# Kernel optimization log

Hardware: AMD Instinct MI355X
Metric: run time of the kernel (lower is better)

The kernel has to match this reference:

```python
import jax, jax.numpy as jnp
import numpy as np

N, F_IN, F_OUT, K = 16384, 64, 64, 3


def setup_inputs() -> dict:
    key = jax.random.key(0)
    k1, k2, k3, k4 = jax.random.split(key, 4)
    x = jax.random.normal(k1, (N, F_IN), dtype=jnp.float32)
    # dense rescaled Laplacian; scale so repeated matmuls stay numerically tame
    L_tilde = jax.random.normal(k2, (N, N), dtype=jnp.float32) / np.float32(np.sqrt(N))
    stdv = 1.0 / np.sqrt(F_OUT)
    weights = jax.random.uniform(k3, (K + 1, F_IN, F_OUT), dtype=jnp.float32,
                                 minval=-stdv, maxval=stdv)
    bias = jax.random.uniform(k4, (F_OUT,), dtype=jnp.float32, minval=-stdv, maxval=stdv)
    return {"x": x, "L_tilde": L_tilde, "weights": weights, "bias": bias}


def reference(x, L_tilde, weights, bias):
    # Chebyshev recurrence: T0 = x, T1 = L@x, Tk = 2*L@T_{k-1} - T_{k-2}
    T_prev = x                                   # (N, F_in)
    out = T_prev @ weights[0]                    # (N, F_out)
    T_curr = L_tilde @ x
    out = out + T_curr @ weights[1]
    for k in range(2, K + 1):                    # fixed small K: python loop is fine
        T_next = 2.0 * (L_tilde @ T_curr) - T_prev
        out = out + T_next @ weights[k]
        T_prev, T_curr = T_curr, T_next
    return out + bias
```

## Files before the change

### kernel.cpp

```cpp
#include <hip/hip_runtime.h>
#include <cstddef>
#include <cstdint>

#define NN 16384
#define FF 64
#define BM 64
#define BK 64
#define SK 4
#define KQ (NN / SK)
#define NC (KQ / BK)

typedef __attribute__((ext_vector_type(8))) short bf16x8;
typedef __attribute__((ext_vector_type(4))) float f32x4;
typedef unsigned short ushort_t;

#define GLOBAL_AS __attribute__((address_space(1)))
#define LDS_AS    __attribute__((address_space(3)))

__device__ __forceinline__ void f32_split(float f, ushort_t& h, ushort_t& l) {
    unsigned u = __builtin_bit_cast(unsigned, f);
    h = (ushort_t)(u >> 16);
    float hf = __builtin_bit_cast(float, u & 0xFFFF0000u);
    float lo = f - hf;
    l = (ushort_t)(__builtin_bit_cast(unsigned, lo) >> 16);
}

__global__ __launch_bounds__(256) void convT_init(
    const float* __restrict__ X, ushort_t* __restrict__ Th,
    ushort_t* __restrict__ Tl, const float* __restrict__ W0,
    const float* __restrict__ bias, float* __restrict__ out)
{
    __shared__ float S[64][68];
    __shared__ float W[64][64];
    const int t = threadIdx.x;
    const int rb = blockIdx.x * 64;
    {
        const int row = t >> 2;
        const int c0 = (t & 3) * 16;
        const float* src = X + (size_t)(rb + row) * FF + c0;
        *(float4*)&S[row][c0 + 0]  = *(const float4*)(src + 0);
        *(float4*)&S[row][c0 + 4]  = *(const float4*)(src + 4);
        *(float4*)&S[row][c0 + 8]  = *(const float4*)(src + 8);
        *(float4*)&S[row][c0 + 12] = *(const float4*)(src + 12);
        float4* wd = (float4*)&W[0][0];
        const float4* ws = (const float4*)W0;
#pragma unroll
        for (int j = 0; j < 4; ++j) wd[t * 4 + j] = ws[t * 4 + j];
    }
    __syncthreads();
    {
        const int cc = t >> 2;
        const int r0 = (t & 3) * 16;
        ushort_t hh[16], ll[16];
#pragma unroll
        for (int i = 0; i < 16; ++i) f32_split(S[r0 + i][cc], hh[i], ll[i]);
        unsigned wh[8], wl[8];
#pragma unroll
        for (int j = 0; j < 8; ++j) {
            wh[j] = (unsigned)hh[2 * j] | ((unsigned)hh[2 * j + 1] << 16);
            wl[j] = (unsigned)ll[2 * j] | ((unsigned)ll[2 * j + 1] << 16);
        }
        const size_t o = (size_t)cc * NN + rb + r0;
        *(uint4*)(Th + o)     = make_uint4(wh[0], wh[1], wh[2], wh[3]);
        *(uint4*)(Th + o + 8) = make_uint4(wh[4], wh[5], wh[6], wh[7]);
        *(uint4*)(Tl + o)     = make_uint4(wl[0], wl[1], wl[2], wl[3]);
        *(uint4*)(Tl + o + 8) = make_uint4(wl[4], wl[5], wl[6], wl[7]);
    }
    {
        const int row0 = (t >> 3) * 2;
        const int col0 = (t & 7) * 8;
        float acc[2][8];
        const float4 b0 = *(const float4*)(bias + col0);
        const float4 b1 = *(const float4*)(bias + col0 + 4);
#pragma unroll
        for (int r = 0; r < 2; ++r) {
            acc[r][0] = b0.x; acc[r][1] = b0.y; acc[r][2] = b0.z; acc[r][3] = b0.w;
            acc[r][4] = b1.x; acc[r][5] = b1.y; acc[r][6] = b1.z; acc[r][7] = b1.w;
        }
#pragma unroll
        for (int f = 0; f < FF; ++f) {
            const float x0 = S[row0][f];
            const float x1 = S[row0 + 1][f];
            const float4 w0 = *(const float4*)&W[f][col0];
            const float4 w1 = *(const float4*)&W[f][col0 + 4];
            acc[0][0] += x0 * w0.x; acc[0][1] += x0 * w0.y;
            acc[0][2] += x0 * w0.z; acc[0][3] += x0 * w0.w;
            acc[0][4] += x0 * w1.x; acc[0][5] += x0 * w1.y;
            acc[0][6] += x0 * w1.z; acc[0][7] += x0 * w1.w;
            acc[1][0] += x1 * w0.x; acc[1][1] += x1 * w0.y;
            acc[1][2] += x1 * w0.z; acc[1][3] += x1 * w0.w;
            acc[1][4] += x1 * w1.x; acc[1][5] += x1 * w1.y;
            acc[1][6] += x1 * w1.z; acc[1][7] += x1 * w1.w;
        }
#pragma unroll
        for (int r = 0; r < 2; ++r) {
            const size_t o = (size_t)(rb + row0 + r) * FF + col0;
            float4 v0, v1;
            v0.x = acc[r][0]; v0.y = acc[r][1]; v0.z = acc[r][2]; v0.w = acc[r][3];
            v1.x = acc[r][4]; v1.y = acc[r][5]; v1.z = acc[r][6]; v1.w = acc[r][7];
            *(float4*)(out + o) = v0;
            *(float4*)(out + o + 4) = v1;
        }
    }
}

__global__ __launch_bounds__(256) void cheb_gemm_mfma(
    const float* __restrict__ L, const ushort_t* __restrict__ Th,
    const ushort_t* __restrict__ Tl, float* __restrict__ P)
{
    __shared__ ushort_t Ah[2][BM * BK];
    __shared__ ushort_t Al[2][BM * BK];
    __shared__ ushort_t Bh[2][FF * BK];
    __shared__ ushort_t Bl[2][FF * BK];

    const int tid  = threadIdx.x;
    const int lane = tid & 63;
    const int w    = tid >> 6;
    const int s    = blockIdx.x >> 8;
    const int m    = blockIdx.x & 255;
    const int row0g = m * BM;
    const int kbase = s * KQ;

    const int wm = w >> 1, wn = w & 1;
    const int frow = lane & 15;
    const int fk8  = (lane >> 4) * 8;

    const int arow = w * 4 + (lane >> 4);
    const int akq  = lane & 15;
    const int axor = (arow & 7) << 4;

    const ushort_t* Tsrc = (w & 1) ? Tl : Th;
    const int boct0 = (w >> 1) * 4;

    f32x4 acc[2][2];
#pragma unroll
    for (int i = 0; i < 2; ++i)
#pragma unroll
        for (int j = 0; j < 2; ++j) acc[i][j] = (f32x4)0.f;

    float4 va[4];

    const float* Labase = L + (size_t)(row0g + arow) * NN + kbase + akq * 4;

#define ISSUE_B(c, slot)                                                        \
    {                                                                           \
        const size_t kc = (size_t)(c) * BK;                                     \
        char* bbase = (char*)((w & 1) ? Bl[slot] : Bh[slot]);                   \
        _Pragma("unroll")                                                       \
        for (int o = 0; o < 4; ++o) {                                           \
            const int oct = boct0 + o;                                          \
            const int col = oct * 8 + (lane >> 3);                              \
            const ushort_t* g = Tsrc + (size_t)col * NN + kbase + kc            \
                                + (((lane & 7) ^ (col & 7)) * 8);               \
            __builtin_amdgcn_global_load_lds((const GLOBAL_AS void*)g,          \
                (LDS_AS void*)(bbase + oct * 1024), 16, 0, 0);                  \
        }                                                                       \
    }

#define LOAD_A(c)                                                               \
    {                                                                           \
        const float* g = Labase + (size_t)(c) * BK;                             \
        va[0] = *(const float4*)(g);                                            \
        va[1] = *(const float4*)(g + (size_t)16 * NN);                          \
        va[2] = *(const float4*)(g + (size_t)32 * NN);                          \
        va[3] = *(const float4*)(g + (size_t)48 * NN);                          \
    }

#define CONV_WRITE_A(slot)                                                      \
    {                                                                           \
        char* ahb = (char*)Ah[slot];                                            \
        char* alb = (char*)Al[slot];                                            \
        _Pragma("unroll")                                                       \
        for (int p = 0; p < 4; ++p) {                                           \
            const int r = arow + p * 16;                                        \
            ushort_t h0, h1, h2, h3, l0, l1, l2, l3;                            \
            f32_split(va[p].x, h0, l0);                                         \
            f32_split(va[p].y, h1, l1);                                         \
            f32_split(va[p].z, h2, l2);                                         \
            f32_split(va[p].w, h3, l3);                                         \
            const unsigned hi01 = (unsigned)h0 | ((unsigned)h1 << 16);          \
            const unsigned hi23 = (unsigned)h2 | ((unsigned)h3 << 16);          \
            const unsigned lo01 = (unsigned)l0 | ((unsigned)l1 << 16);          \
            const unsigned lo23 = (unsigned)l2 | ((unsigned)l3 << 16);          \
            const int byte = (r * 128 + akq * 8) ^ axor;                        \
            *(uint2*)(ahb + byte) = make_uint2(hi01, hi23);                     \
            *(uint2*)(alb + byte) = make_uint2(lo01, lo23);                     \
        }                                                                       \
    }

    ISSUE_B(0, 0)
    LOAD_A(0)
    CONV_WRITE_A(0)
    __syncthreads();

    for (int c = 0; c < NC; ++c) {
        const int slot = c & 1;
        if (c + 1 < NC) {
            ISSUE_B(c + 1, slot ^ 1)
            LOAD_A(c + 1)
        }
        {
            const char* ahb = (const char*)Ah[slot];
            const char* alb = (const char*)Al[slot];
            const char* bhb = (const char*)Bh[slot];
            const char* blb = (const char*)Bl[slot];
#pragma unroll
            for (int ks = 0; ks < 2; ++ks) {
                const int kk = ks * 32 + fk8;
                bf16x8 Afh[2], Afl[2], Bfh[2], Bfl[2];
#pragma unroll
                for (int mt = 0; mt < 2; ++mt) {
                    const int row = wm * 32 + mt * 16 + frow;
                    const int off = (row * 128 + kk * 2) ^ ((row & 7) << 4);
                    Afh[mt] = *(const bf16x8*)(ahb + off);
                    Afl[mt] = *(const bf16x8*)(alb + off);
                }
#pragma unroll
                for (int nt = 0; nt < 2; ++nt) {
                    const int col = wn * 32 + nt * 16 + frow;
                    const int off = (col * 128 + kk * 2) ^ ((col & 7) << 4);
                    Bfh[nt] = *(const bf16x8*)(bhb + off);
                    Bfl[nt] = *(const bf16x8*)(blb + off);
                }
#pragma unroll
                for (int mt = 0; mt < 2; ++mt)
#pragma unroll
                    for (int nt = 0; nt < 2; ++nt) {
                        acc[mt][nt] = __builtin_amdgcn_mfma_f32_16x16x32_bf16(
                            Afh[mt], Bfh[nt], acc[mt][nt], 0, 0, 0);
                        acc[mt][nt] = __builtin_amdgcn_mfma_f32_16x16x32_bf16(
                            Afh[mt], Bfl[nt], acc[mt][nt], 0, 0, 0);
                        acc[mt][nt] = __builtin_amdgcn_mfma_f32_16x16x32_bf16(
                            Afl[mt], Bfh[nt], acc[mt][nt], 0, 0, 0);
                    }
            }
        }
        if (c + 1 < NC) CONV_WRITE_A(slot ^ 1)
        __syncthreads();
    }

    float* Pp = P + (size_t)s * NN * FF;
#pragma unroll
    for (int mt = 0; mt < 2; ++mt)
#pragma unroll
        for (int nt = 0; nt < 2; ++nt) {
            const int row = row0g + wm * 32 + mt * 16 + (lane >> 4) * 4;
            const int col = wn * 32 + nt * 16 + frow;
#pragma unroll
            for (int r = 0; r < 4; ++r)
                Pp[(size_t)(row + r) * FF + col] = acc[mt][nt][r];
        }
#undef ISSUE_B
#undef LOAD_A
#undef CONV_WRITE_A
}

__global__ __launch_bounds__(256) void post_hop(
    const float* __restrict__ P,
    const float* __restrict__ Tsub, const float* __restrict__ Wk,
    float* __restrict__ Tstore, ushort_t* __restrict__ Thn,
    ushort_t* __restrict__ Tln, float* __restrict__ out,
    float alpha, float beta)
{
    __shared__ float ST[64][33];
    __shared__ float WK[64][64];
    const int t = threadIdx.x;
    const int rb = blockIdx.x * 32;
    const size_t M1 = (size_t)NN * FF;

    {
        float4* wd = (float4*)&WK[0][0];
        const float4* ws = (const float4*)Wk;
#pragma unroll
        for (int j = 0; j < 4; ++j) wd[t * 4 + j] = ws[t * 4 + j];
    }

    const int row = t >> 3;
    const int c0 = (t & 7) * 8;
    const size_t o = (size_t)(rb + row) * FF + c0;

    {
        float tv[8];
#pragma unroll
        for (int half = 0; half < 2; ++half) {
            const size_t oo = o + 4 * half;
            float4 a0 = *(const float4*)(P + oo);
            const float4 a1 = *(const float4*)(P + M1 + oo);
            const float4 a2 = *(const float4*)(P + 2 * M1 + oo);
            const float4 a3 = *(const float4*)(P + 3 * M1 + oo);
            a0.x += a1.x + a2.x + a3.x; a0.y += a1.y + a2.y + a3.y;
            a0.z += a1.z + a2.z + a3.z; a0.w += a1.w + a2.w + a3.w;
            tv[4 * half + 0] = alpha * a0.x; tv[4 * half + 1] = alpha * a0.y;
            tv[4 * half + 2] = alpha * a0.z; tv[4 * half + 3] = alpha * a0.w;
        }
        if (beta != 0.f) {
            const float4 s0 = *(const float4*)(Tsub + o);
            const float4 s1 = *(const float4*)(Tsub + o + 4);
            tv[0] += beta * s0.x; tv[1] += beta * s0.y;
            tv[2] += beta * s0.z; tv[3] += beta * s0.w;
            tv[4] += beta * s1.x; tv[5] += beta * s1.y;
            tv[6] += beta * s1.z; tv[7] += beta * s1.w;
        }
        if (Tstore) {
            float4 v0, v1;
            v0.x = tv[0]; v0.y = tv[1]; v0.z = tv[2]; v0.w = tv[3];
            v1.x = tv[4]; v1.y = tv[5]; v1.z = tv[6]; v1.w = tv[7];
            *(float4*)(Tstore + o) = v0;
            *(float4*)(Tstore + o + 4) = v1;
        }
#pragma unroll
        for (int j = 0; j < 8; ++j) ST[c0 + j][row] = tv[j];
    }
    __syncthreads();

    if (Thn) {
        const int f = t >> 2;
        const int r0 = (t & 3) * 8;
        ushort_t hh[8], ll[8];
#pragma unroll
        for (int i = 0; i < 8; ++i) f32_split(ST[f][r0 + i], hh[i], ll[i]);
        unsigned wh[4], wl[4];
#pragma unroll
        for (int j = 0; j < 4; ++j) {
            wh[j] = (unsigned)hh[2 * j] | ((unsigned)hh[2 * j + 1] << 16);
            wl[j] = (unsigned)ll[2 * j] | ((unsigned)ll[2 * j + 1] << 16);
        }
        const size_t ob = (size_t)f * NN + rb + r0;
        *(uint4*)(Thn + ob) = make_uint4(wh[0], wh[1], wh[2], wh[3]);
        *(uint4*)(Tln + ob) = make_uint4(wl[0], wl[1], wl[2], wl[3]);
    }

    {
        float4 a0 = *(const float4*)(out + o);
        float4 a1 = *(const float4*)(out + o + 4);
#pragma unroll
        for (int f = 0; f < FF; ++f) {
            const float sv = ST[f][row];
            const float4 w0 = *(const float4*)&WK[f][c0];
            const float4 w1 = *(const float4*)&WK[f][c0 + 4];
            a0.x += sv * w0.x; a0.y += sv * w0.y;
            a0.z += sv * w0.z; a0.w += sv * w0.w;
            a1.x += sv * w1.x; a1.y += sv * w1.y;
            a1.z += sv * w1.z; a1.w += sv * w1.w;
        }
        *(float4*)(out + o) = a0;
        *(float4*)(out + o + 4) = a1;
    }
}

extern "C" void kernel_launch(void* const* d_in, const int* in_sizes, int n_in,
                              void* d_out, int out_size, void* d_ws, size_t ws_size,
                              hipStream_t stream)
{
    const float* x    = (const float*)d_in[0];
    const float* L    = (const float*)d_in[1];
    const float* W    = (const float*)d_in[2];
    const float* bias = (const float*)d_in[3];
    float* out = (float*)d_out;

    const size_t M1 = (size_t)NN * FF;
    float* wsf = (float*)d_ws;
    float* T1 = wsf;
    float* P  = wsf + M1;
    ushort_t* ThA = (ushort_t*)(wsf + 5 * M1);
    ushort_t* TlA = ThA + M1;
    ushort_t* ThB = TlA + M1;
    ushort_t* TlB = ThB + M1;

    const dim3 gc(NN / 64), bc(256);
    const dim3 gg(SK * 256), bg(256);
    const dim3 gp(NN / 32), bp(256);

    convT_init<<<gc, bc, 0, stream>>>(x, ThA, TlA, W + 0 * FF * FF, bias, out);
    cheb_gemm_mfma<<<gg, bg, 0, stream>>>(L, ThA, TlA, P);
    post_hop<<<gp, bp, 0, stream>>>(P, x, W + 1 * FF * FF,
                                    T1, ThB, TlB, out, 1.f, 0.f);
    cheb_gemm_mfma<<<gg, bg, 0, stream>>>(L, ThB, TlB, P);
    post_hop<<<gp, bp, 0, stream>>>(P, x, W + 2 * FF * FF,
                                    nullptr, ThA, TlA, out, 2.f, -1.f);
    cheb_gemm_mfma<<<gg, bg, 0, stream>>>(L, ThA, TlA, P);
    post_hop<<<gp, bp, 0, stream>>>(P, T1, W + 3 * FF * FF,
                                    nullptr, nullptr, nullptr, out, 2.f, -1.f);
}
```

Baseline: 725.9 us.

## Halve K-tile depth to 32 and re-layout LDS swizzle for A and B

Reduces the K chunk per pipeline stage from 64 to 32, which halves LDS tiles per stage (and LDS use, possibly raising occupancy). A loads switch to two contiguous float4 per thread per row with a new 4-way XOR swizzle, B async loads are remapped to match, and the compute loop loses its inner ks loop. The cost is twice as many iterations and barriers, with fewer bytes in flight per stage to hide memory latency on this memory-bound L stream.

```diff
diff --git a/kernel.cpp b/kernel.cpp
--- a/kernel.cpp
+++ b/kernel.cpp
@@ -5,7 +5,7 @@
 #define NN 16384
 #define FF 64
 #define BM 64
-#define BK 64
+#define BK 32
 #define SK 4
 #define KQ (NN / SK)
 #define NC (KQ / BK)
@@ -123,11 +123,11 @@
 
     const int wm = w >> 1, wn = w & 1;
     const int frow = lane & 15;
-    const int fk8  = (lane >> 4) * 8;
-
-    const int arow = w * 4 + (lane >> 4);
-    const int akq  = lane & 15;
-    const int axor = (arow & 7) << 4;
+    const int fkq  = lane >> 4;
+
+    const int ar  = tid >> 2;
+    const int akq = tid & 3;
+    const int abyte = ar * 64 + ((akq ^ (ar & 3)) << 4);
 
     const ushort_t* Tsrc = (w & 1) ? Tl : Th;
     const int boct0 = (w >> 1) * 4;
@@ -138,54 +138,86 @@
 #pragma unroll
         for (int j = 0; j < 2; ++j) acc[i][j] = (f32x4)0.f;
 
-    float4 va[4];
-
-    const float* Labase = L + (size_t)(row0g + arow) * NN + kbase + akq * 4;
+    float4 va0, va1;
+
+    const float* Labase = L + (size_t)(row0g + ar) * NN + kbase + akq * 8;
 
 #define ISSUE_B(c, slot)                                                        \
     {                                                                           \
         const size_t kc = (size_t)(c) * BK;                                     \
         char* bbase = (char*)((w & 1) ? Bl[slot] : Bh[slot]);                   \
         _Pragma("unroll")                                                       \
-        for (int o = 0; o < 4; ++o) {                                           \
-            const int oct = boct0 + o;                                          \
-            const int col = oct * 8 + (lane >> 3);                              \
-            const ushort_t* g = Tsrc + (size_t)col * NN + kbase + kc            \
-                                + (((lane & 7) ^ (col & 7)) * 8);               \
+        for (int j = 0; j < 2; ++j) {                                           \
+            const int oct2 = boct0 + 2 * j;                   \
+            const int col = oct2 * 8 + (lane >> 5) * 8 + ((lane & 31) >> 2);    \
+            const int sg = (lane & 3) ^ (col & 3);                              \
+            const ushort_t* g = Tsrc + (size_t)col * NN + kbase + kc + sg * 8;  \
             __builtin_amdgcn_global_load_lds((const GLOBAL_AS void*)g,          \
-                (LDS_AS void*)(bbase + oct * 1024), 16, 0, 0);                  \
+                (LDS_AS void*)(bbase + oct2 * 512), 16, 0, 0);                  \
         }                                                                       \
     }
 
 #define LOAD_A(c)                                                               \
     {                                                                           \
         const float* g = Labase + (size_t)(c) * BK;                             \
-        va[0] = *(const float4*)(g);                                            \
-        va[1] = *(const float4*)(g + (size_t)16 * NN);                          \
-        va[2] = *(const float4*)(g + (size_t)32 * NN);                          \
-        va[3] = *(const float4*)(g + (size_t)48 * NN);                          \
+        va0 = *(const float4*)(g);                                              \
+        va1 = *(const float4*)(g + 4);                                          \
     }
 
 #define CONV_WRITE_A(slot)                                                      \
     {                                                                           \
-        char* ahb = (char*)Ah[slot];                                            \
-        char* alb = (char*)Al[slot];                                            \
+        ushort_t h0, h1, h2, h3, l0, l1, l2, l3;                                \
+        ushort_t h4, h5, h6, h7, l4, l5, l6, l7;                                \
+        f32_split(va0.x, h0, l0); f32_split(va0.y, h1, l1);                     \
+        f32_split(va0.z, h2, l2); f32_split(va0.w, h3, l3);                     \
+        f32_split(va1.x, h4, l4); f32_split(va1.y, h5, l5);                     \
+        f32_split(va1.z, h6, l6); f32_split(va1.w, h7, l7);                     \
+        const uint4 hv = make_uint4(                                            \
+            (unsigned)h0 | ((unsigned)h1 << 16),                                \
+            (unsigned)h2 | ((unsigned)h3 << 16),                                \
+            (unsigned)h4 | ((unsigned)h5 << 16),                                \
+            (unsigned)h6 | ((unsigned)h7 << 16));                               \
+        const uint4 lv = make_uint4(                                            \
+            (unsigned)l0 | ((unsigned)l1 << 16),                                \
+            (unsigned)l2 | ((unsigned)l3 << 16),                                \
+            (unsigned)l4 | ((unsigned)l5 << 16),                                \
+            (unsigned)l6 | ((unsigned)l7 << 16));                               \
+        *(uint4*)((char*)Ah[slot] + abyte) = hv;                                \
+        *(uint4*)((char*)Al[slot] + abyte) = lv;                                \
+    }
+
+#define COMPUTE(slot)                                                           \
+    {                                                                           \
+        const char* ahb = (const char*)Ah[slot];                                \
+        const char* alb = (const char*)Al[slot];                                \
+        const char* bhb = (const char*)Bh[slot];                                \
+        const char* blb = (const char*)Bl[slot];                                \
+        bf16x8 Afh[2], Afl[2], Bfh[2], Bfl[2];                                  \
         _Pragma("unroll")                                                       \
-        for (int p = 0; p < 4; ++p) {                                           \
-            const int r = arow + p * 16;                                        \
-            ushort_t h0, h1, h2, h3, l0, l1, l2, l3;                            \
-            f32_split(va[p].x, h0, l0);                                         \
-            f32_split(va[p].y, h1, l1);                                         \
-            f32_split(va[p].z, h2, l2);                                         \
-            f32_split(va[p].w, h3, l3);                                         \
-            const unsigned hi01 = (unsigned)h0 | ((unsigned)h1 << 16);          \
-            const unsigned hi23 = (unsigned)h2 | ((unsigned)h3 << 16);          \
-            const unsigned lo01 = (unsigned)l0 | ((unsigned)l1 << 16);          \
-            const unsigned lo23 = (unsigned)l2 | ((unsigned)l3 << 16);          \
-            const int byte = (r * 128 + akq * 8) ^ axor;                        \
-            *(uint2*)(ahb + byte) = make_uint2(hi01, hi23);                     \
-            *(uint2*)(alb + byte) = make_uint2(lo01, lo23);                     \
+        for (int mt = 0; mt < 2; ++mt) {                                        \
+            const int row = wm * 32 + mt * 16 + frow;                           \
+            const int off = row * 64 + ((fkq ^ (row & 3)) << 4);                \
+            Afh[mt] = *(const bf16x8*)(ahb + off);                              \
+            Afl[mt] = *(const bf16x8*)(alb + off);                              \
         }                                                                       \
+        _Pragma("unroll")                                                       \
+        for (int nt = 0; nt < 2; ++nt) {                                        \
+            const int col = wn * 32 + nt * 16 + frow;                           \
+            const int off = col * 64 + ((fkq ^ (col & 3)) << 4);                \
+            Bfh[nt] = *(const bf16x8*)(bhb + off);                              \
+            Bfl[nt] = *(const bf16x8*)(blb + off);                              \
+        }                                                                       \
+        _Pragma("unroll")                                                       \
+        for (int mt = 0; mt < 2; ++mt)                                          \
+            _Pragma("unroll")                                                   \
+            for (int nt = 0; nt < 2; ++nt) {                                    \
+                acc[mt][nt] = __builtin_amdgcn_mfma_f32_16x16x32_bf16(          \
+                    Afh[mt], Bfh[nt], acc[mt][nt], 0, 0, 0);                    \
+                acc[mt][nt] = __builtin_amdgcn_mfma_f32_16x16x32_bf16(          \
+                    Afh[mt], Bfl[nt], acc[mt][nt], 0, 0, 0);                    \
+                acc[mt][nt] = __builtin_amdgcn_mfma_f32_16x16x32_bf16(          \
+                    Afl[mt], Bfh[nt], acc[mt][nt], 0, 0, 0);                    \
+            }                                                                   \
     }
 
     ISSUE_B(0, 0)
@@ -193,48 +225,14 @@
     CONV_WRITE_A(0)
     __syncthreads();
 
+#pragma unroll 1
     for (int c = 0; c < NC; ++c) {
         const int slot = c & 1;
         if (c + 1 < NC) {
             ISSUE_B(c + 1, slot ^ 1)
             LOAD_A(c + 1)
         }
-        {
-            const char* ahb = (const char*)Ah[slot];
-            const char* alb = (const char*)Al[slot];
-            const char* bhb = (const char*)Bh[slot];
-            const char* blb = (const char*)Bl[slot];
-#pragma unroll
-            for (int ks = 0; ks < 2; ++ks) {
-                const int kk = ks * 32 + fk8;
-                bf16x8 Afh[2], Afl[2], Bfh[2], Bfl[2];
-#pragma unroll
-                for (int mt = 0; mt < 2; ++mt) {
-                    const int row = wm * 32 + mt * 16 + frow;
-                    const int off = (row * 128 + kk * 2) ^ ((row & 7) << 4);
-                    Afh[mt] = *(const bf16x8*)(ahb + off);
-                    Afl[mt] = *(const bf16x8*)(alb + off);
-                }
-#pragma unroll
-                for (int nt = 0; nt < 2; ++nt) {
-                    const int col = wn * 32 + nt * 16 + frow;
-                    const int off = (col * 128 + kk * 2) ^ ((col & 7) << 4);
-                    Bfh[nt] = *(const bf16x8*)(bhb + off);
-                    Bfl[nt] = *(const bf16x8*)(blb + off);
-                }
-#pragma unroll
-                for (int mt = 0; mt < 2; ++mt)
-#pragma unroll
-                    for (int nt = 0; nt < 2; ++nt) {
-                        acc[mt][nt] = __builtin_amdgcn_mfma_f32_16x16x32_bf16(
-                            Afh[mt], Bfh[nt], acc[mt][nt], 0, 0, 0);
-                        acc[mt][nt] = __builtin_amdgcn_mfma_f32_16x16x32_bf16(
-                            Afh[mt], Bfl[nt], acc[mt][nt], 0, 0, 0);
-                        acc[mt][nt] = __builtin_amdgcn_mfma_f32_16x16x32_bf16(
-                            Afl[mt], Bfh[nt], acc[mt][nt], 0, 0, 0);
-                    }
-            }
-        }
+        COMPUTE(slot)
         if (c + 1 < NC) CONV_WRITE_A(slot ^ 1)
         __syncthreads();
     }
@@ -253,6 +251,7 @@
 #undef ISSUE_B
 #undef LOAD_A
 #undef CONV_WRITE_A
+#undef COMPUTE
 }
 
 __global__ __launch_bounds__(256) void post_hop(
```

Result: slower. 773.1 us (+6.5%).

## Deepen GEMM pipeline with two-chunk prefetch and triple-buffered B tiles

Applied to the files above, without the earlier changes.

Restructures the cheb_gemm main loop to keep two K-chunks of loads in flight: A fragments go through two register sets and B tiles are triple-buffered in LDS. Synchronisation uses explicit vmcnt/lgkmcnt waits, raw s_barrier and sched_barrier fences in place of __syncthreads. The aim is to hide global-load latency of the large L matrix behind the MFMA work. In exchange it uses more LDS and registers, and the correctness of the hand-placed wait counts is delicate.

```diff
diff --git a/kernel.cpp b/kernel.cpp
--- a/kernel.cpp
+++ b/kernel.cpp
@@ -16,6 +16,12 @@
 
 #define GLOBAL_AS __attribute__((address_space(1)))
 #define LDS_AS    __attribute__((address_space(3)))
+
+#define VMCNT8   asm volatile("s_waitcnt vmcnt(8)" ::: "memory")
+#define VMCNT0   asm volatile("s_waitcnt vmcnt(0)" ::: "memory")
+#define LGKMCNT0 asm volatile("s_waitcnt lgkmcnt(0)" ::: "memory")
+#define SCHEDB   __builtin_amdgcn_sched_barrier(0)
+#define BARRIER  __builtin_amdgcn_s_barrier()
 
 __device__ __forceinline__ void f32_split(float f, ushort_t& h, ushort_t& l) {
     unsigned u = __builtin_bit_cast(unsigned, f);
@@ -110,8 +116,8 @@
 {
     __shared__ ushort_t Ah[2][BM * BK];
     __shared__ ushort_t Al[2][BM * BK];
-    __shared__ ushort_t Bh[2][FF * BK];
-    __shared__ ushort_t Bl[2][FF * BK];
+    __shared__ ushort_t Bh[3][FF * BK];
+    __shared__ ushort_t Bl[3][FF * BK];
 
     const int tid  = threadIdx.x;
     const int lane = tid & 63;
@@ -138,14 +144,14 @@
 #pragma unroll
         for (int j = 0; j < 2; ++j) acc[i][j] = (f32x4)0.f;
 
-    float4 va[4];
+    float4 vaA[4], vaB[4];
 
     const float* Labase = L + (size_t)(row0g + arow) * NN + kbase + akq * 4;
 
-#define ISSUE_B(c, slot)                                                        \
+#define ISSUE_B(c, sb)                                                          \
     {                                                                           \
         const size_t kc = (size_t)(c) * BK;                                     \
-        char* bbase = (char*)((w & 1) ? Bl[slot] : Bh[slot]);                   \
+        char* bbase = (char*)((w & 1) ? Bl[sb] : Bh[sb]);                       \
         _Pragma("unroll")                                                       \
         for (int o = 0; o < 4; ++o) {                                           \
             const int oct = boct0 + o;                                          \
@@ -157,7 +163,7 @@
         }                                                                       \
     }
 
-#define LOAD_A(c)                                                               \
+#define LOAD_A(va, c)                                                           \
     {                                                                           \
         const float* g = Labase + (size_t)(c) * BK;                             \
         va[0] = *(const float4*)(g);                                            \
@@ -166,10 +172,10 @@
         va[3] = *(const float4*)(g + (size_t)48 * NN);                          \
     }
 
-#define CONV_WRITE_A(slot)                                                      \
+#define CONV_WRITE_A(va, sa)                                                    \
     {                                                                           \
-        char* ahb = (char*)Ah[slot];                                            \
-        char* alb = (char*)Al[slot];                                            \
+        char* ahb = (char*)Ah[sa];                                              \
+        char* alb = (char*)Al[sa];                                              \
         _Pragma("unroll")                                                       \
         for (int p = 0; p < 4; ++p) {                                           \
             const int r = arow + p * 16;                                        \
@@ -188,55 +194,85 @@
         }                                                                       \
     }
 
+#define COMPUTE(sa, sb)                                                         \
+    {                                                                           \
+        const char* ahb = (const char*)Ah[sa];                                  \
+        const char* alb = (const char*)Al[sa];                                  \
+        const char* bhb = (const char*)Bh[sb];                                  \
+        const char* blb = (const char*)Bl[sb];                                  \
+        _Pragma("unroll")                                                       \
+        for (int ks = 0; ks < 2; ++ks) {                                        \
+            const int kk = ks * 32 + fk8;                                       \
+            bf16x8 Afh[2], Afl[2], Bfh[2], Bfl[2];                              \
+            _Pragma("unroll")                                                   \
+            for (int mt = 0; mt < 2; ++mt) {                                    \
+                const int row = wm * 32 + mt * 16 + frow;                       \
+                const int off = (row * 128 + kk * 2) ^ ((row & 7) << 4);        \
+                Afh[mt] = *(const bf16x8*)(ahb + off);                          \
+                Afl[mt] = *(const bf16x8*)(alb + off);                          \
+            }                                                                   \
+            _Pragma("unroll")                                                   \
+            for (int nt = 0; nt < 2; ++nt) {                                    \
+                const int col = wn * 32 + nt * 16 + frow;                       \
+                const int off = (col * 128 + kk * 2) ^ ((col & 7) << 4);        \
+                Bfh[nt] = *(const bf16x8*)(bhb + off);                          \
+                Bfl[nt] = *(const bf16x8*)(blb + off);                          \
+            }                                                                   \
+            _Pragma("unroll")                                                   \
+            for (int mt = 0; mt < 2; ++mt)                                      \
+                _Pragma("unroll")                                               \
+                for (int nt = 0; nt < 2; ++nt) {                                \
+                    acc[mt][nt] = __builtin_amdgcn_mfma_f32_16x16x32_bf16(      \
+                        Afh[mt], Bfh[nt], acc[mt][nt], 0, 0, 0);                \
+                    acc[mt][nt] = __builtin_amdgcn_mfma_f32_16x16x32_bf16(      \
+                        Afh[mt], Bfl[nt], acc[mt][nt], 0, 0, 0);                \
+                    acc[mt][nt] = __builtin_amdgcn_mfma_f32_16x16x32_bf16(      \
+                        Afl[mt], Bfh[nt], acc[mt][nt], 0, 0, 0);                \
+                }                                                               \
+        }                                                                       \
+    }
+
+    LOAD_A(vaA, 0)
     ISSUE_B(0, 0)
-    LOAD_A(0)
-    CONV_WRITE_A(0)
-    __syncthreads();
-
-    for (int c = 0; c < NC; ++c) {
-        const int slot = c & 1;
-        if (c + 1 < NC) {
-            ISSUE_B(c + 1, slot ^ 1)
-            LOAD_A(c + 1)
-        }
-        {
-            const char* ahb = (const char*)Ah[slot];
-            const char* alb = (const char*)Al[slot];
-            const char* bhb = (const char*)Bh[slot];
-            const char* blb = (const char*)Bl[slot];
-#pragma unroll
-            for (int ks = 0; ks < 2; ++ks) {
-                const int kk = ks * 32 + fk8;
-                bf16x8 Afh[2], Afl[2], Bfh[2], Bfl[2];
-#pragma unroll
-                for (int mt = 0; mt < 2; ++mt) {
-                    const int row = wm * 32 + mt * 16 + frow;
-                    const int off = (row * 128 + kk * 2) ^ ((row & 7) << 4);
-                    Afh[mt] = *(const bf16x8*)(ahb + off);
-                    Afl[mt] = *(const bf16x8*)(alb + off);
-                }
-#pragma unroll
-                for (int nt = 0; nt < 2; ++nt) {
-                    const int col = wn * 32 + nt * 16 + frow;
-                    const int off = (col * 128 + kk * 2) ^ ((col & 7) << 4);
-                    Bfh[nt] = *(const bf16x8*)(bhb + off);
-                    Bfl[nt] = *(const bf16x8*)(blb + off);
-                }
-#pragma unroll
-                for (int mt = 0; mt < 2; ++mt)
-#pragma unroll
-                    for (int nt = 0; nt < 2; ++nt) {
-                        acc[mt][nt] = __builtin_amdgcn_mfma_f32_16x16x32_bf16(
-                            Afh[mt], Bfh[nt], acc[mt][nt], 0, 0, 0);
-                        acc[mt][nt] = __builtin_amdgcn_mfma_f32_16x16x32_bf16(
-                            Afh[mt], Bfl[nt], acc[mt][nt], 0, 0, 0);
-                        acc[mt][nt] = __builtin_amdgcn_mfma_f32_16x16x32_bf16(
-                            Afl[mt], Bfh[nt], acc[mt][nt], 0, 0, 0);
-                    }
-            }
-        }
-        if (c + 1 < NC) CONV_WRITE_A(slot ^ 1)
-        __syncthreads();
+    LOAD_A(vaB, 1)
+    ISSUE_B(1, 1)
+    SCHEDB;
+    VMCNT8;
+    SCHEDB;
+    CONV_WRITE_A(vaA, 0)
+    LGKMCNT0;
+    BARRIER;
+    SCHEDB;
+
+#pragma unroll 1
+    for (int c = 0; c < NC; c += 2) {
+        if (c + 2 < NC) {
+            LOAD_A(vaA, c + 2)
+            ISSUE_B(c + 2, (c + 2) % 3)
+            SCHEDB;
+        }
+        COMPUTE(0, c % 3)
+        if (c + 2 < NC) { VMCNT8; } else { VMCNT0; }
+        SCHEDB;
+        CONV_WRITE_A(vaB, 1)
+        LGKMCNT0;
+        BARRIER;
+        SCHEDB;
+
+        if (c + 3 < NC) {
+            LOAD_A(vaB, c + 3)
+            ISSUE_B(c + 3, (c + 3) % 3)
+            SCHEDB;
+        }
+        COMPUTE(1, (c + 1) % 3)
+        if (c + 2 < NC) {
+            if (c + 3 < NC) { VMCNT8; } else { VMCNT0; }
+            SCHEDB;
+            CONV_WRITE_A(vaA, 0)
+            LGKMCNT0;
+            BARRIER;
+            SCHEDB;
+        }
     }
 
     float* Pp = P + (size_t)s * NN * FF;
@@ -253,6 +289,7 @@
 #undef ISSUE_B
 #undef LOAD_A
 #undef CONV_WRITE_A
+#undef COMPUTE
 }
 
 __global__ __launch_bounds__(256) void post_hop(
```

Result: slower. 763.8 us (+5.2%).
